# Optimization experiments

Hardware: AMD Instinct MI355X
Metric: run time of the kernel (lower is better)

## Reference

```python
import jax, jax.numpy as jnp
import numpy as np

B, LQ, LK, D, H = 8, 1024, 1024, 1024, 16
HD = D // H  # 64


def setup_inputs() -> dict:
    key = jax.random.key(0)
    ks = jax.random.split(key, 8)
    s = 0.02  # weight init scale
    return {
        "q_in": jax.random.normal(ks[0], (B, LQ, D), jnp.float32),
        "k_in": jax.random.normal(ks[1], (B, LK, D), jnp.float32),
        "v_in": jax.random.normal(ks[2], (B, LK, D), jnp.float32),
        "wq": jax.random.normal(ks[3], (D, D), jnp.float32) * s,
        "bq": jnp.zeros((D,), jnp.float32),
        "wk": jax.random.normal(ks[4], (D, D), jnp.float32) * s,
        "bk": jnp.zeros((D,), jnp.float32),
        "wv": jax.random.normal(ks[5], (D, D), jnp.float32) * s,
        "bv": jnp.zeros((D,), jnp.float32),
        "wo": jax.random.normal(ks[6], (D, D), jnp.float32) * s,
        "bo": jnp.zeros((D,), jnp.float32),
        # is_masked=True buffer: tril of ones -> True on lower triangle (masked-out positions, per original masked_fill semantics)
        "mask": jnp.tril(jnp.ones((LQ, LK), jnp.bool_)),
    }


def reference(q_in, k_in, v_in, wq, bq, wk, bk, wv, bv, wo, bo, mask):
    # torch Linear: x @ W.T + b
    q = (q_in @ wq.T + bq).reshape(B, H, LQ, HD)  # plain view, as in original
    k = (k_in @ wk.T + bk).reshape(B, H, LK, HD)
    v = (v_in @ wv.T + bv).reshape(B, H, LK, HD)
    # QUIRK: original scales by sqrt(query.size(1)) == sqrt(head_num), not sqrt(head_dim)
    scale = jnp.sqrt(jnp.float32(H))
    h = jnp.einsum("bhik,bhjk->bhij", q, k) / scale  # [B,H,LQ,LK]
    # masked_fill(-inf) then nan_to_num (maps -inf -> finfo.min, matching torch defaults)
    h = jnp.nan_to_num(jnp.where(mask, -jnp.inf, h))
    w = jax.nn.softmax(h, axis=-1)
    heads = jnp.einsum("bhij,bhjv->bhiv", w, v).reshape(B, LQ, H * HD)
    return heads @ wo.T + bo
```

## Files before the change

### kernel.cpp

```cpp
#include <hip/hip_runtime.h>
#include <hip/hip_bf16.h>

typedef __bf16 bf16;
typedef _Float16 f16;
typedef __attribute__((ext_vector_type(8))) __bf16 bf16x8;
typedef __attribute__((ext_vector_type(4))) __bf16 bf16x4;
typedef __attribute__((ext_vector_type(8))) _Float16 f16x8;
typedef __attribute__((ext_vector_type(4))) _Float16 f16x4;
typedef __attribute__((ext_vector_type(4))) float f32x4;

#define BB 8
#define SEQ 1024
#define DD 1024
#define HDIM 64
#define CHUNK 65536
#define MROWS (BB * SEQ)
#define NE_IN 8388608
#define NE_W  1048576

__device__ __forceinline__ void async_load16(const bf16* g, bf16* l) {
  __builtin_amdgcn_global_load_lds(
      (const __attribute__((address_space(1))) void*)g,
      (__attribute__((address_space(3))) void*)l, 16, 0, 0);
}

struct CvtArgs {
  const float* src[7];
  bf16* dst[7];
  int n[7];
};
__global__ __launch_bounds__(256) void cvt_bf16(CvtArgs a) {
  const int t = blockIdx.y;
  const long idx = ((long)blockIdx.x * 256 + threadIdx.x) * 8;
  if (idx >= a.n[t]) return;
  const float* s = a.src[t] + idx;
  f32x4 x = *(const f32x4*)s;
  f32x4 y = *(const f32x4*)(s + 4);
  bf16x8 o;
  o[0] = (bf16)x[0]; o[1] = (bf16)x[1]; o[2] = (bf16)x[2]; o[3] = (bf16)x[3];
  o[4] = (bf16)y[0]; o[5] = (bf16)y[1]; o[6] = (bf16)y[2]; o[7] = (bf16)y[3];
  *(bf16x8*)(a.dst[t] + idx) = o;
}

__global__ __launch_bounds__(256) void gemm_qkv(
    const bf16* __restrict__ Abase, const bf16* __restrict__ Wbase,
    const float* __restrict__ bq, const float* __restrict__ bk,
    const float* __restrict__ bv, bf16* __restrict__ Obase)
{
  __shared__ __attribute__((aligned(16))) bf16 As[128 * 32];
  __shared__ __attribute__((aligned(16))) bf16 Bs[128 * 32];

  const int tid  = threadIdx.x;
  const int lane = tid & 63;
  const int wid  = tid >> 6;
  const int wm   = wid >> 1, wn = wid & 1;
  const int quad = lane >> 4, l15 = lane & 15;
  const int m0 = blockIdx.x * 128;
  const int n0 = blockIdx.y * 128;
  const int t  = n0 >> 10;

  const bf16* A = Abase + (size_t)t * NE_IN;
  const float* bias = (t == 0) ? bq : (t == 1) ? bk : bv;
  const float scale = (t == 0) ? 0.25f : 1.0f;
  bf16* Cout = Obase + (size_t)t * NE_IN;
  const int nc0 = n0 & 1023;

  f32x4 acc[4][4];
#pragma unroll
  for (int i = 0; i < 4; i++)
#pragma unroll
    for (int j = 0; j < 4; j++) acc[i][j] = f32x4{0.f, 0.f, 0.f, 0.f};

  const int srow = wid * 16 + (lane >> 2);
  const int scol = (lane & 3) * 8;
  const bf16* gA = A + (size_t)(m0 + srow) * DD + scol;
  const bf16* gB = Wbase + (size_t)(n0 + srow) * DD + scol;
  bf16* lA = As + wid * 512;
  bf16* lB = Bs + wid * 512;

  for (int k0 = 0; k0 < DD; k0 += 32) {
    async_load16(gA + k0,           lA);
    async_load16(gA + k0 + 64 * DD, lA + 2048);
    async_load16(gB + k0,           lB);
    async_load16(gB + k0 + 64 * DD, lB + 2048);
    __syncthreads();

    bf16x8 af[4], bfr[4];
#pragma unroll
    for (int mi = 0; mi < 4; mi++)
      af[mi] = *(const bf16x8*)&As[(wm * 64 + mi * 16 + l15) * 32 + quad * 8];
#pragma unroll
    for (int ni = 0; ni < 4; ni++)
      bfr[ni] = *(const bf16x8*)&Bs[(wn * 64 + ni * 16 + l15) * 32 + quad * 8];
#pragma unroll
    for (int mi = 0; mi < 4; mi++)
#pragma unroll
      for (int ni = 0; ni < 4; ni++)
        acc[mi][ni] = __builtin_amdgcn_mfma_f32_16x16x32_bf16(
            af[mi], bfr[ni], acc[mi][ni], 0, 0, 0);
    __syncthreads();
  }

#pragma unroll
  for (int mi = 0; mi < 4; mi++) {
#pragma unroll
    for (int ni = 0; ni < 4; ni++) {
      const int col = nc0 + wn * 64 + ni * 16 + l15;
      const float bv_ = bias[col];
#pragma unroll
      for (int r = 0; r < 4; r++) {
        const int row = m0 + wm * 64 + mi * 16 + quad * 4 + r;
        Cout[(size_t)row * DD + col] = (bf16)((acc[mi][ni][r] + bv_) * scale);
      }
    }
  }
}

__global__ __launch_bounds__(256) void gemm_out(
    const bf16* __restrict__ A, const bf16* __restrict__ Bw,
    const float* __restrict__ bias, float* __restrict__ Cout)
{
  __shared__ __attribute__((aligned(16))) bf16 As[128 * 32];
  __shared__ __attribute__((aligned(16))) bf16 Bs[128 * 32];

  const int tid  = threadIdx.x;
  const int lane = tid & 63;
  const int wid  = tid >> 6;
  const int wm   = wid >> 1, wn = wid & 1;
  const int quad = lane >> 4, l15 = lane & 15;
  const int m0 = blockIdx.x * 128;
  const int n0 = blockIdx.y * 128;

  f32x4 acc[4][4];
#pragma unroll
  for (int i = 0; i < 4; i++)
#pragma unroll
    for (int j = 0; j < 4; j++) acc[i][j] = f32x4{0.f, 0.f, 0.f, 0.f};

  const int srow = wid * 16 + (lane >> 2);
  const int scol = (lane & 3) * 8;
  const bf16* gA = A  + (size_t)(m0 + srow) * DD + scol;
  const bf16* gB = Bw + (size_t)(n0 + srow) * DD + scol;
  bf16* lA = As + wid * 512;
  bf16* lB = Bs + wid * 512;

  for (int k0 = 0; k0 < DD; k0 += 32) {
    async_load16(gA + k0,           lA);
    async_load16(gA + k0 + 64 * DD, lA + 2048);
    async_load16(gB + k0,           lB);
    async_load16(gB + k0 + 64 * DD, lB + 2048);
    __syncthreads();

    bf16x8 af[4], bfr[4];
#pragma unroll
    for (int mi = 0; mi < 4; mi++)
      af[mi] = *(const bf16x8*)&As[(wm * 64 + mi * 16 + l15) * 32 + quad * 8];
#pragma unroll
    for (int ni = 0; ni < 4; ni++)
      bfr[ni] = *(const bf16x8*)&Bs[(wn * 64 + ni * 16 + l15) * 32 + quad * 8];
#pragma unroll
    for (int mi = 0; mi < 4; mi++)
#pragma unroll
      for (int ni = 0; ni < 4; ni++)
        acc[mi][ni] = __builtin_amdgcn_mfma_f32_16x16x32_bf16(
            af[mi], bfr[ni], acc[mi][ni], 0, 0, 0);
    __syncthreads();
  }

#pragma unroll
  for (int mi = 0; mi < 4; mi++) {
#pragma unroll
    for (int ni = 0; ni < 4; ni++) {
      const int col = n0 + wn * 64 + ni * 16 + l15;
      const float bv_ = bias[col];
#pragma unroll
      for (int r = 0; r < 4; r++) {
        const int row = m0 + wm * 64 + mi * 16 + quad * 4 + r;
        Cout[(size_t)row * DD + col] = acc[mi][ni][r] + bv_;
      }
    }
  }
}

__global__ __launch_bounds__(256) void vtrans(
    const bf16* __restrict__ V, f16* __restrict__ Vt)
{
  __shared__ __attribute__((aligned(16))) bf16 T[64][72];
  const int tid = threadIdx.x;
  const int r  = tid >> 2;
  const int c0 = (tid & 3) * 16;
  const size_t base = (size_t)blockIdx.y * CHUNK;
  const int kv0 = blockIdx.x * 64;

  const bf16* src = V + base + (size_t)(kv0 + r) * HDIM + c0;
  *(bf16x8*)&T[r][c0]     = *(const bf16x8*)src;
  *(bf16x8*)&T[r][c0 + 8] = *(const bf16x8*)(src + 8);
  __syncthreads();

  f16x8 o0, o1;
#pragma unroll
  for (int j = 0; j < 8; j++) {
    o0[j] = (f16)(float)T[c0 + j][r];
    o1[j] = (f16)(float)T[c0 + 8 + j][r];
  }
  f16* dst = Vt + base + (size_t)r * SEQ + kv0 + c0;
  *(f16x8*)dst       = o0;
  *(f16x8*)(dst + 8) = o1;
}

__global__ __launch_bounds__(256) void attn5(
    const bf16* __restrict__ Q, const bf16* __restrict__ K,
    const f16* __restrict__ Vt, bf16* __restrict__ O)
{
  __shared__ __attribute__((aligned(16))) bf16 Ks[64][72];
  __shared__ __attribute__((aligned(16))) f16  Vs[64][72];

  const int tid  = threadIdx.x;
  const int lane = tid & 63;
  const int wid  = tid >> 6;
  const int quad = lane >> 4, l15 = lane & 15;
  const int q0   = blockIdx.y * 64;
  const size_t base = (size_t)blockIdx.x * CHUNK;
  const int qg = q0 + wid * 16 + l15;

  bf16x8 qb[2];
#pragma unroll
  for (int ks = 0; ks < 2; ks++)
    qb[ks] = *(const bf16x8*)&Q[base + (size_t)qg * HDIM + ks * 32 + quad * 8];

  f32x4 oacc[4];
#pragma unroll
  for (int h = 0; h < 4; h++) oacc[h] = f32x4{0.f, 0.f, 0.f, 0.f};
  float lsum = 0.f;

  const int sr = tid >> 2;
  const int sc = (tid & 3) * 16;
  const bf16* gK = K + base + (size_t)sr * HDIM + sc;
  const f16*  gV = Vt + base + (size_t)sr * SEQ + sc;

  const int kv_begin = (q0 == SEQ - 64) ? 0 : q0;

  for (int kv0 = kv_begin; kv0 < SEQ; kv0 += 64) {
    {
      const bf16* pk = gK + (size_t)kv0 * HDIM;
      *(bf16x8*)&Ks[sr][sc]     = *(const bf16x8*)pk;
      *(bf16x8*)&Ks[sr][sc + 8] = *(const bf16x8*)(pk + 8);
      const f16* pv = gV + kv0;
      *(f16x8*)&Vs[sr][sc]     = *(const f16x8*)pv;
      *(f16x8*)&Vs[sr][sc + 8] = *(const f16x8*)(pv + 8);
    }
    __syncthreads();

#pragma unroll
    for (int t = 0; t < 4; t++) {
      f32x4 s = f32x4{0.f, 0.f, 0.f, 0.f};
#pragma unroll
      for (int ks = 0; ks < 2; ks++) {
        bf16x8 kf = *(const bf16x8*)&Ks[t * 16 + l15][ks * 32 + quad * 8];
        s = __builtin_amdgcn_mfma_f32_16x16x32_bf16(kf, qb[ks], s, 0, 0, 0);
      }
      f16x4 pf;
#pragma unroll
      for (int r = 0; r < 4; r++) {
        const int kvg = kv0 + t * 16 + quad * 4 + r;
        float p;
        if (kvg <= qg) p = (qg == SEQ - 1) ? 1.0f : 0.0f;
        else           p = __expf(s[r]);
        const f16 ph = (f16)p;
        pf[r] = ph;
        lsum += (float)ph;
      }
#pragma unroll
      for (int h = 0; h < 4; h++) {
        f16x4 vf = *(const f16x4*)&Vs[h * 16 + l15][t * 16 + quad * 4];
        oacc[h] = __builtin_amdgcn_mfma_f32_16x16x16f16(vf, pf, oacc[h], 0, 0, 0);
      }
    }
    __syncthreads();
  }

  lsum += __shfl_xor(lsum, 16);
  lsum += __shfl_xor(lsum, 32);
  const float rinv = 1.0f / lsum;

#pragma unroll
  for (int h = 0; h < 4; h++) {
    bf16x4 w;
#pragma unroll
    for (int r = 0; r < 4; r++) w[r] = (bf16)(oacc[h][r] * rinv);
    *(bf16x4*)&Ks[wid * 16 + l15][h * 16 + quad * 4] = w;
  }
  __syncthreads();
  {
    const int row = tid >> 2;
    const int c   = (tid & 3) * 16;
    bf16* dst = O + base + (size_t)(q0 + row) * HDIM + c;
    *(bf16x8*)dst       = *(const bf16x8*)&Ks[row][c];
    *(bf16x8*)(dst + 8) = *(const bf16x8*)&Ks[row][c + 8];
  }
}

extern "C" void kernel_launch(void* const* d_in, const int* in_sizes, int n_in,
                              void* d_out, int out_size, void* d_ws, size_t ws_size,
                              hipStream_t stream) {
  (void)in_sizes; (void)n_in; (void)out_size; (void)ws_size;
  const float* q_in = (const float*)d_in[0];
  const float* k_in = (const float*)d_in[1];
  const float* v_in = (const float*)d_in[2];
  const float* wq   = (const float*)d_in[3];
  const float* bq   = (const float*)d_in[4];
  const float* wk   = (const float*)d_in[5];
  const float* bk   = (const float*)d_in[6];
  const float* wv   = (const float*)d_in[7];
  const float* bv   = (const float*)d_in[8];
  const float* wo   = (const float*)d_in[9];
  const float* bo   = (const float*)d_in[10];

  bf16* wqb  = (bf16*)d_ws;
  bf16* wkb  = wqb + NE_W;
  bf16* wvb  = wkb + NE_W;
  bf16* wob  = wvb + NE_W;
  bf16* qinb = wob + NE_W;
  bf16* kinb = qinb + NE_IN;
  bf16* vinb = kinb + NE_IN;
  bf16* Qb   = vinb + NE_IN;
  bf16* Kb   = Qb + NE_IN;
  bf16* Vb   = Kb + NE_IN;
  f16*  VtG  = (f16*)qinb;
  bf16* Hb   = kinb;

  CvtArgs ca;
  ca.src[0] = q_in; ca.dst[0] = qinb; ca.n[0] = NE_IN;
  ca.src[1] = k_in; ca.dst[1] = kinb; ca.n[1] = NE_IN;
  ca.src[2] = v_in; ca.dst[2] = vinb; ca.n[2] = NE_IN;
  ca.src[3] = wq;   ca.dst[3] = wqb;  ca.n[3] = NE_W;
  ca.src[4] = wk;   ca.dst[4] = wkb;  ca.n[4] = NE_W;
  ca.src[5] = wv;   ca.dst[5] = wvb;  ca.n[5] = NE_W;
  ca.src[6] = wo;   ca.dst[6] = wob;  ca.n[6] = NE_W;
  cvt_bf16<<<dim3(NE_IN / 2048, 7), 256, 0, stream>>>(ca);

  gemm_qkv<<<dim3(MROWS / 128, 3 * DD / 128), 256, 0, stream>>>(
      qinb, wqb, bq, bk, bv, Qb);

  vtrans<<<dim3(SEQ / 64, BB * 16), 256, 0, stream>>>(Vb, VtG);
  attn5<<<dim3(BB * 16, SEQ / 64), 256, 0, stream>>>(Qb, Kb, VtG, Hb);

  gemm_out<<<dim3(MROWS / 128, DD / 128), 256, 0, stream>>>(
      Hb, wob, bo, (float*)d_out);
}
```

Baseline: 331.2 us.

## Process two query tiles per attention block and compute row sums with MFMA

Each attention block now handles 128 query rows as two 64-row subtiles sharing one K/V tile load, so each staged K/V tile is reused for twice as many queries. Fully masked kv tiles are skipped per subtile, and exp is replaced by exp2 with log2(e) folded into the Q projection scale. The softmax denominator is accumulated by an MFMA against a vector of ones instead of scalar sums and cross-lane shuffles. This cuts K/V global traffic and transcendental cost, but raises register pressure and halves the grid, which may reduce occupancy and worsen load balance across the causal triangle.

```diff
diff --git a/kernel.cpp b/kernel.cpp
--- a/kernel.cpp
+++ b/kernel.cpp
@@ -17,6 +17,8 @@
 #define MROWS (BB * SEQ)
 #define NE_IN 8388608
 #define NE_W  1048576
+
+#define QSCALE 0.3606737602222409f
 
 __device__ __forceinline__ void async_load16(const bf16* g, bf16* l) {
   __builtin_amdgcn_global_load_lds(
@@ -61,7 +63,7 @@
 
   const bf16* A = Abase + (size_t)t * NE_IN;
   const float* bias = (t == 0) ? bq : (t == 1) ? bk : bv;
-  const float scale = (t == 0) ? 0.25f : 1.0f;
+  const float scale = (t == 0) ? QSCALE : 1.0f;
   bf16* Cout = Obase + (size_t)t * NE_IN;
   const int nc0 = n0 & 1023;
 
@@ -208,7 +210,7 @@
   *(f16x8*)(dst + 8) = o1;
 }
 
-__global__ __launch_bounds__(256) void attn5(
+__global__ __launch_bounds__(256) void attn6(
     const bf16* __restrict__ Q, const bf16* __restrict__ K,
     const f16* __restrict__ Vt, bf16* __restrict__ O)
 {
@@ -219,26 +221,39 @@
   const int lane = tid & 63;
   const int wid  = tid >> 6;
   const int quad = lane >> 4, l15 = lane & 15;
-  const int q0   = blockIdx.y * 64;
+  const int q0   = blockIdx.y * 128;
   const size_t base = (size_t)blockIdx.x * CHUNK;
-  const int qg = q0 + wid * 16 + l15;
-
-  bf16x8 qb[2];
-#pragma unroll
-  for (int ks = 0; ks < 2; ks++)
-    qb[ks] = *(const bf16x8*)&Q[base + (size_t)qg * HDIM + ks * 32 + quad * 8];
-
-  f32x4 oacc[4];
-#pragma unroll
-  for (int h = 0; h < 4; h++) oacc[h] = f32x4{0.f, 0.f, 0.f, 0.f};
-  float lsum = 0.f;
+
+  const int sA = q0 + wid * 16;
+  const int sB = sA + 64;
+  const int qgA = sA + l15;
+  const int qgB = sB + l15;
+
+  bf16x8 qbA[2], qbB[2];
+#pragma unroll
+  for (int ks = 0; ks < 2; ks++) {
+    qbA[ks] = *(const bf16x8*)&Q[base + (size_t)qgA * HDIM + ks * 32 + quad * 8];
+    qbB[ks] = *(const bf16x8*)&Q[base + (size_t)qgB * HDIM + ks * 32 + quad * 8];
+  }
+
+  f32x4 oaccA[4], oaccB[4], laccA, laccB;
+#pragma unroll
+  for (int h = 0; h < 4; h++) {
+    oaccA[h] = f32x4{0.f, 0.f, 0.f, 0.f};
+    oaccB[h] = f32x4{0.f, 0.f, 0.f, 0.f};
+  }
+  laccA = f32x4{0.f, 0.f, 0.f, 0.f};
+  laccB = f32x4{0.f, 0.f, 0.f, 0.f};
+  const f16x4 ones = f16x4{(f16)1.f, (f16)1.f, (f16)1.f, (f16)1.f};
 
   const int sr = tid >> 2;
   const int sc = (tid & 3) * 16;
-  const bf16* gK = K + base + (size_t)sr * HDIM + sc;
-  const f16*  gV = Vt + base + (size_t)sr * SEQ + sc;
-
-  const int kv_begin = (q0 == SEQ - 64) ? 0 : q0;
+  const bf16* gK = K  + base + (size_t)sr * HDIM + sc;
+  const f16*  gV = Vt + base + (size_t)sr * SEQ  + sc;
+
+  const bool lastBlk = (q0 == SEQ - 128);
+  const int kv_begin = lastBlk ? 0 : q0;
+  const bool uniRow = lastBlk && (wid == 3);
 
   for (int kv0 = kv_begin; kv0 < SEQ; kv0 += 64) {
     {
@@ -251,43 +266,80 @@
     }
     __syncthreads();
 
+    const bool activeA = (kv0 + 63 > sA);
+    const bool activeB = (kv0 + 63 > sB);
+
 #pragma unroll
     for (int t = 0; t < 4; t++) {
-      f32x4 s = f32x4{0.f, 0.f, 0.f, 0.f};
-#pragma unroll
-      for (int ks = 0; ks < 2; ks++) {
-        bf16x8 kf = *(const bf16x8*)&Ks[t * 16 + l15][ks * 32 + quad * 8];
-        s = __builtin_amdgcn_mfma_f32_16x16x32_bf16(kf, qb[ks], s, 0, 0, 0);
+      bf16x8 kf0 = *(const bf16x8*)&Ks[t * 16 + l15][quad * 8];
+      bf16x8 kf1 = *(const bf16x8*)&Ks[t * 16 + l15][32 + quad * 8];
+      f16x4 vf[4];
+#pragma unroll
+      for (int h = 0; h < 4; h++)
+        vf[h] = *(const f16x4*)&Vs[h * 16 + l15][t * 16 + quad * 4];
+
+      if (activeA) {
+        f32x4 s = f32x4{0.f, 0.f, 0.f, 0.f};
+        s = __builtin_amdgcn_mfma_f32_16x16x32_bf16(kf0, qbA[0], s, 0, 0, 0);
+        s = __builtin_amdgcn_mfma_f32_16x16x32_bf16(kf1, qbA[1], s, 0, 0, 0);
+        f16x4 pf;
+        if (kv0 + t * 16 <= sA + 15) {
+#pragma unroll
+          for (int r = 0; r < 4; r++) {
+            const int kvg = kv0 + t * 16 + quad * 4 + r;
+            const float p = (kvg <= qgA) ? 0.f : __builtin_amdgcn_exp2f(s[r]);
+            pf[r] = (f16)p;
+          }
+        } else {
+#pragma unroll
+          for (int r = 0; r < 4; r++) pf[r] = (f16)__builtin_amdgcn_exp2f(s[r]);
+        }
+        laccA = __builtin_amdgcn_mfma_f32_16x16x16f16(ones, pf, laccA, 0, 0, 0);
+#pragma unroll
+        for (int h = 0; h < 4; h++)
+          oaccA[h] = __builtin_amdgcn_mfma_f32_16x16x16f16(vf[h], pf, oaccA[h], 0, 0, 0);
       }
-      f16x4 pf;
-#pragma unroll
-      for (int r = 0; r < 4; r++) {
-        const int kvg = kv0 + t * 16 + quad * 4 + r;
-        float p;
-        if (kvg <= qg) p = (qg == SEQ - 1) ? 1.0f : 0.0f;
-        else           p = __expf(s[r]);
-        const f16 ph = (f16)p;
-        pf[r] = ph;
-        lsum += (float)ph;
-      }
-#pragma unroll
-      for (int h = 0; h < 4; h++) {
-        f16x4 vf = *(const f16x4*)&Vs[h * 16 + l15][t * 16 + quad * 4];
-        oacc[h] = __builtin_amdgcn_mfma_f32_16x16x16f16(vf, pf, oacc[h], 0, 0, 0);
+
+      if (activeB) {
+        f32x4 s = f32x4{0.f, 0.f, 0.f, 0.f};
+        s = __builtin_amdgcn_mfma_f32_16x16x32_bf16(kf0, qbB[0], s, 0, 0, 0);
+        s = __builtin_amdgcn_mfma_f32_16x16x32_bf16(kf1, qbB[1], s, 0, 0, 0);
+        f16x4 pf;
+        if (kv0 + t * 16 <= sB + 15) {
+#pragma unroll
+          for (int r = 0; r < 4; r++) {
+            const int kvg = kv0 + t * 16 + quad * 4 + r;
+            const float p = (kvg <= qgB) ? ((qgB == SEQ - 1) ? 1.f : 0.f)
+                                         : __builtin_amdgcn_exp2f(s[r]);
+            pf[r] = (f16)p;
+          }
+        } else {
+#pragma unroll
+          for (int r = 0; r < 4; r++) pf[r] = (f16)__builtin_amdgcn_exp2f(s[r]);
+        }
+        laccB = __builtin_amdgcn_mfma_f32_16x16x16f16(ones, pf, laccB, 0, 0, 0);
+#pragma unroll
+        for (int h = 0; h < 4; h++)
+          oaccB[h] = __builtin_amdgcn_mfma_f32_16x16x16f16(vf[h], pf, oaccB[h], 0, 0, 0);
+      } else if (uniRow) {
+        f16x4 pf = (l15 == 15) ? ones : f16x4{(f16)0.f, (f16)0.f, (f16)0.f, (f16)0.f};
+        laccB = __builtin_amdgcn_mfma_f32_16x16x16f16(ones, pf, laccB, 0, 0, 0);
+#pragma unroll
+        for (int h = 0; h < 4; h++)
+          oaccB[h] = __builtin_amdgcn_mfma_f32_16x16x16f16(vf[h], pf, oaccB[h], 0, 0, 0);
       }
     }
     __syncthreads();
   }
 
-  lsum += __shfl_xor(lsum, 16);
-  lsum += __shfl_xor(lsum, 32);
-  const float rinv = 1.0f / lsum;
+  const float rinvA = 1.0f / laccA[0];
+  const float rinvB = 1.0f / laccB[0];
 
 #pragma unroll
   for (int h = 0; h < 4; h++) {
     bf16x4 w;
 #pragma unroll
-    for (int r = 0; r < 4; r++) w[r] = (bf16)(oacc[h][r] * rinv);
+    for (int r = 0; r < 4; r++) w[r] = (bf16)(oaccA[h][r] * rinvA);
     *(bf16x4*)&Ks[wid * 16 + l15][h * 16 + quad * 4] = w;
   }
   __syncthreads();
@@ -295,6 +347,22 @@
     const int row = tid >> 2;
     const int c   = (tid & 3) * 16;
     bf16* dst = O + base + (size_t)(q0 + row) * HDIM + c;
+    *(bf16x8*)dst       = *(const bf16x8*)&Ks[row][c];
+    *(bf16x8*)(dst + 8) = *(const bf16x8*)&Ks[row][c + 8];
+  }
+  __syncthreads();
+#pragma unroll
+  for (int h = 0; h < 4; h++) {
+    bf16x4 w;
+#pragma unroll
+    for (int r = 0; r < 4; r++) w[r] = (bf16)(oaccB[h][r] * rinvB);
+    *(bf16x4*)&Ks[wid * 16 + l15][h * 16 + quad * 4] = w;
+  }
+  __syncthreads();
+  {
+    const int row = tid >> 2;
+    const int c   = (tid & 3) * 16;
+    bf16* dst = O + base + (size_t)(q0 + 64 + row) * HDIM + c;
     *(bf16x8*)dst       = *(const bf16x8*)&Ks[row][c];
     *(bf16x8*)(dst + 8) = *(const bf16x8*)&Ks[row][c + 8];
   }
@@ -343,7 +411,7 @@
       qinb, wqb, bq, bk, bv, Qb);
 
   vtrans<<<dim3(SEQ / 64, BB * 16), 256, 0, stream>>>(Vb, VtG);
-  attn5<<<dim3(BB * 16, SEQ / 64), 256, 0, stream>>>(Qb, Kb, VtG, Hb);
+  attn6<<<dim3(BB * 16, SEQ / 128), 256, 0, stream>>>(Qb, Kb, VtG, Hb);
 
   gemm_out<<<dim3(MROWS / 128, DD / 128), 256, 0, stream>>>(
       Hb, wob, bo, (float*)d_out);
```

Result: faster. 313.2 us (-5.4%).
